# Optimization experiments

Measured on AMD Instinct MI355X. Metric: run time of the kernel, lower is better.

Reference implementation:

```python
import jax, jax.numpy as jnp
import numpy as np
import math

N, D, H, N_BINS, MAX_GRID = 4096, 512, 4, 32, 40

def setup_inputs() -> dict:
    key = jax.random.key(0)
    ks = jax.random.split(key, 12)
    vision_h = jax.random.normal(ks[0], (N, D), dtype=jnp.float32)
    patch_rows = jax.random.randint(ks[1], (N,), 0, MAX_GRID, dtype=jnp.int32)
    patch_cols = jax.random.randint(ks[2], (N,), 0, MAX_GRID, dtype=jnp.int32)
    pos_w = 0.01 * jax.random.normal(ks[3], (D, D), dtype=jnp.float32)
    q_w = 0.02 * jax.random.normal(ks[4], (D, D), dtype=jnp.float32)
    k_w = 0.02 * jax.random.normal(ks[5], (D, D), dtype=jnp.float32)
    v_w = 0.02 * jax.random.normal(ks[6], (D, D), dtype=jnp.float32)
    out_w = 0.02 * jax.random.normal(ks[7], (D, D), dtype=jnp.float32)
    dist_bias = 0.02 * jax.random.normal(ks[8], (H, N_BINS), dtype=jnp.float32)
    gamma_param = jnp.array(0.5, dtype=jnp.float32)
    ln_w = jnp.ones((D,), dtype=jnp.float32)
    ln_b = jnp.zeros((D,), dtype=jnp.float32)
    return {"vision_h": vision_h, "patch_rows": patch_rows, "patch_cols": patch_cols,
            "pos_w": pos_w, "q_w": q_w, "k_w": k_w, "v_w": v_w, "out_w": out_w,
            "dist_bias": dist_bias, "gamma_param": gamma_param, "ln_w": ln_w, "ln_b": ln_b}

def _sin_pe_1d(pos_f, half_dim):
    # pos_f: (N,) float. returns (N, half_dim) with even idx = sin, odd idx = cos
    freq = jnp.exp(jnp.arange(0, half_dim, 2, dtype=jnp.float32) * (-(math.log(10000.0) / half_dim)))
    ang = pos_f[:, None] * freq  # (N, half_dim//2)
    return jnp.stack([jnp.sin(ang), jnp.cos(ang)], axis=-1).reshape(pos_f.shape[0], half_dim)

def reference(vision_h, patch_rows, patch_cols, pos_w, q_w, k_w, v_w, out_w,
              dist_bias, gamma_param, ln_w, ln_b):
    n, d = vision_h.shape
    h = dist_bias.shape[0]
    hd = d // h
    n_bins = dist_bias.shape[1]
    half = d // 2

    rows_f = patch_rows.astype(jnp.float32)
    cols_f = patch_cols.astype(jnp.float32)
    pe = jnp.concatenate([_sin_pe_1d(rows_f, half), _sin_pe_1d(cols_f, half)], axis=-1)  # (N, D)

    h_pos = vision_h + pe @ pos_w.T
    Q = (h_pos @ q_w.T).reshape(n, h, hd).transpose(1, 0, 2)   # (H, N, hd)
    K = (h_pos @ k_w.T).reshape(n, h, hd).transpose(1, 0, 2)
    V = (vision_h @ v_w.T).reshape(n, h, hd).transpose(1, 0, 2)

    logits = jnp.einsum("hnd,hmd->hnm", Q, K) / math.sqrt(hd)   # (H, N, N)

    row_diff = rows_f[:, None] - rows_f[None, :]
    col_diff = cols_f[:, None] - cols_f[None, :]
    dist = jnp.sqrt(row_diff ** 2 + col_diff ** 2)              # (N, N)
    max_log_dist = math.log1p(MAX_GRID * math.sqrt(2.0))
    bins = (jnp.log1p(dist) / max_log_dist * (n_bins - 1)).astype(jnp.int32)
    bins = jnp.clip(bins, 0, n_bins - 1)
    rel_bias = dist_bias[:, bins]                               # (H, N, N)

    attn = jax.nn.softmax(logits + rel_bias, axis=-1)
    attn_out = jnp.einsum("hnm,hmd->hnd", attn, V).transpose(1, 0, 2).reshape(n, d)

    o = attn_out @ out_w.T
    mu = jnp.mean(o, axis=-1, keepdims=True)
    var = jnp.mean((o - mu) ** 2, axis=-1, keepdims=True)
    o_ln = (o - mu) / jnp.sqrt(var + 1e-5) * ln_w + ln_b

    gamma = jax.nn.softplus(gamma_param)
    return vision_h + gamma * o_ln
```

## Files before the change

### kernel.cpp

```cpp
#include <hip/hip_runtime.h>
#include <math.h>

#define N_TOK 4096
#define DMODEL 512
#define NHEAD 4
#define HDIM 128
#define NBINS 32
#define BQ 128
#define BK 64
#define NSPLIT 4
#define KV_PER_SPLIT (N_TOK / NSPLIT)
#define QKSTR 1024
#define LOG2E 1.4426950408889634f

typedef __attribute__((ext_vector_type(8))) short bf16x8;
typedef __attribute__((ext_vector_type(4))) float f32x4;
typedef __attribute__((ext_vector_type(8))) unsigned short u16x8;
typedef __attribute__((ext_vector_type(4))) unsigned short u16x4;

__device__ __forceinline__ unsigned short f2bf(float x) {
    unsigned int u = __float_as_uint(x);
    u += 0x7FFFu + ((u >> 16) & 1u);
    return (unsigned short)(u >> 16);
}
__device__ __forceinline__ float bf2f(unsigned short u) {
    return __uint_as_float(((unsigned int)u) << 16);
}

__global__ __launch_bounds__(256) void pe_prep(const int* __restrict__ rows,
                                               const int* __restrict__ cols,
                                               const float* __restrict__ vh,
                                               unsigned short* __restrict__ pe_bf,
                                               unsigned short* __restrict__ vh_bf) {
    int n = blockIdx.x, t = threadIdx.x;
    float pos = (float)((t < 128) ? rows[n] : cols[n]);
    int k = t & 127;
    float freq = expf(-0.035977892078032f * (float)(2 * k));
    float ang = pos * freq;
    int base = n * DMODEL + ((t < 128) ? 0 : 256) + 2 * k;
    pe_bf[base]     = f2bf(sinf(ang));
    pe_bf[base + 1] = f2bf(cosf(ang));
    float2 v = *(const float2*)&vh[(size_t)n * DMODEL + t * 2];
    vh_bf[(size_t)n * DMODEL + t * 2]     = f2bf(v.x);
    vh_bf[(size_t)n * DMODEL + t * 2 + 1] = f2bf(v.y);
}

__global__ __launch_bounds__(256) void wconv5(const float* __restrict__ w0, const float* __restrict__ w1,
                                              const float* __restrict__ w2, const float* __restrict__ w3,
                                              const float* __restrict__ w4,
                                              unsigned short* __restrict__ dstbase) {
    const float* srcs[5] = {w0, w1, w2, w3, w4};
    const float* src = srcs[blockIdx.y];
    unsigned short* dst = dstbase + (size_t)blockIdx.y * DMODEL * DMODEL;
    int idx = (blockIdx.x * 256 + threadIdx.x) * 4;
    float4 v = *(const float4*)&src[idx];
    u16x4 r;
    r[0] = f2bf(v.x); r[1] = f2bf(v.y); r[2] = f2bf(v.z); r[3] = f2bf(v.w);
    *(u16x4*)&dst[idx] = r;
}

template <bool ADD, bool BF16OUT>
__global__ __launch_bounds__(256) void gemm_mfma(const unsigned short* __restrict__ A,
                                                 const unsigned short* __restrict__ B,
                                                 const float* __restrict__ addv,
                                                 void* __restrict__ Cv,
                                                 int M, int N, int K,
                                                 float scaleA, float scaleB) {
    const int n0 = blockIdx.x * 64;
    const int j0 = blockIdx.y * 128;
    __shared__ unsigned short As[64][72];
    __shared__ unsigned short Bs[128][72];
    const int t    = threadIdx.x;
    const int wid  = t >> 6;
    const int wr   = wid >> 1, wc = wid & 1;
    const int lane = t & 63;
    const int lg   = lane >> 4, li = lane & 15;
    const int str  = t >> 3;
    const int sc   = (t & 7) * 8;

    f32x4 acc[2][4];
#pragma unroll
    for (int i = 0; i < 2; ++i)
#pragma unroll
        for (int j = 0; j < 4; ++j) acc[i][j] = (f32x4){0.f, 0.f, 0.f, 0.f};

    u16x8 areg[2], breg[4];
#pragma unroll
    for (int i = 0; i < 2; ++i)
        areg[i] = *(const u16x8*)&A[(size_t)(n0 + str + i * 32) * K + sc];
#pragma unroll
    for (int i = 0; i < 4; ++i)
        breg[i] = *(const u16x8*)&B[(size_t)(j0 + str + i * 32) * K + sc];

    for (int k0 = 0; k0 < K; k0 += 64) {
        __syncthreads();
#pragma unroll
        for (int i = 0; i < 2; ++i) *(u16x8*)&As[str + i * 32][sc] = areg[i];
#pragma unroll
        for (int i = 0; i < 4; ++i) *(u16x8*)&Bs[str + i * 32][sc] = breg[i];
        __syncthreads();
        if (k0 + 64 < K) {
#pragma unroll
            for (int i = 0; i < 2; ++i)
                areg[i] = *(const u16x8*)&A[(size_t)(n0 + str + i * 32) * K + k0 + 64 + sc];
#pragma unroll
            for (int i = 0; i < 4; ++i)
                breg[i] = *(const u16x8*)&B[(size_t)(j0 + str + i * 32) * K + k0 + 64 + sc];
        }
        __builtin_amdgcn_s_setprio(1);
#pragma unroll
        for (int kc = 0; kc < 2; ++kc) {
            bf16x8 af[2], bfr[4];
#pragma unroll
            for (int mf = 0; mf < 2; ++mf)
                af[mf] = *(const bf16x8*)&As[wr * 32 + mf * 16 + li][kc * 32 + lg * 8];
#pragma unroll
            for (int nf = 0; nf < 4; ++nf)
                bfr[nf] = *(const bf16x8*)&Bs[wc * 64 + nf * 16 + li][kc * 32 + lg * 8];
#pragma unroll
            for (int mf = 0; mf < 2; ++mf)
#pragma unroll
                for (int nf = 0; nf < 4; ++nf)
                    acc[mf][nf] = __builtin_amdgcn_mfma_f32_16x16x32_bf16(af[mf], bfr[nf], acc[mf][nf], 0, 0, 0);
        }
        __builtin_amdgcn_s_setprio(0);
    }
    const float scl = (j0 < 512) ? scaleA : scaleB;
#pragma unroll
    for (int mf = 0; mf < 2; ++mf) {
#pragma unroll
        for (int r = 0; r < 4; ++r) {
            const int row = n0 + wr * 32 + mf * 16 + lg * 4 + r;
#pragma unroll
            for (int nf = 0; nf < 4; ++nf) {
                const int col = j0 + wc * 64 + nf * 16 + li;
                float v = acc[mf][nf][r] * scl;
                if (ADD) v += addv[(size_t)row * N + col];
                if (BF16OUT) ((unsigned short*)Cv)[(size_t)row * N + col] = f2bf(v);
                else         ((float*)Cv)[(size_t)row * N + col] = v;
            }
        }
    }
}

__global__ __launch_bounds__(512, 2) void attn_mfma(const unsigned short* __restrict__ Qb,
                                                    const unsigned short* __restrict__ Kb,
                                                    const unsigned short* __restrict__ Vtb,
                                                    const int* __restrict__ prows,
                                                    const int* __restrict__ pcols,
                                                    const float* __restrict__ dist_bias,
                                                    unsigned short* __restrict__ Opart,
                                                    float* __restrict__ Mp,
                                                    float* __restrict__ Lp) {
    const int h  = blockIdx.y;
    const int n0 = blockIdx.x * BQ;
    const int sp = blockIdx.z;
    __shared__ unsigned short Ks[BK * HDIM];
    __shared__ unsigned short Vts[HDIM * BK];
    __shared__ unsigned short Ps[BQ][68];
    __shared__ unsigned short biasTb[6241];
    __shared__ int klins[BK];

    const int t    = threadIdx.x;
    const int lane = t & 63;
    const int lg   = lane >> 4;
    const int li   = lane & 15;
    const int qbase = (t >> 6) * 16;

    for (int idx = t; idx < 6241; idx += 512) {
        int dr = idx / 79 - 39;
        int dc = idx % 79 - 39;
        float d  = sqrtf((float)(dr * dr + dc * dc));
        int bin  = (int)(log1pf(d) * (31.0f / 4.0529789877f));
        bin = bin > 31 ? 31 : bin;
        biasTb[idx] = f2bf(dist_bias[h * NBINS + bin] * LOG2E);
    }

    bf16x8 qf[4];
    {
        const unsigned short* qptr = &Qb[(size_t)(n0 + qbase + li) * QKSTR + h * HDIM];
#pragma unroll
        for (int kc = 0; kc < 4; ++kc)
            qf[kc] = *(const bf16x8*)&qptr[kc * 32 + lg * 8];
    }
    const int qlin3 = prows[n0 + qbase + li] * 79 + pcols[n0 + qbase + li] + 3120;

    float m_ = -1e30f;
    float l_ = 0.f;
    f32x4 accO[8];
#pragma unroll
    for (int dt = 0; dt < 8; ++dt) accO[dt] = (f32x4){0.f, 0.f, 0.f, 0.f};

    u16x8 kreg[2], vreg[2];
    int klinreg = 0;
    const int ktr = t >> 4, kch = (t & 15) * 8;
    const int vtr = t >> 3, vch = (t & 7) * 8;

    const int kwofs0 = (ktr * 128 + kch) * 2;
    const int vwofs0 = (vtr * 64 + vch) * 2;

    int m0 = sp * KV_PER_SPLIT;
    {
#pragma unroll
        for (int i = 0; i < 2; ++i)
            kreg[i] = *(const u16x8*)&Kb[(size_t)(m0 + ktr + i * 32) * QKSTR + h * HDIM + kch];
#pragma unroll
        for (int i = 0; i < 2; ++i)
            vreg[i] = *(const u16x8*)&Vtb[(size_t)(h * HDIM + vtr + i * 64) * N_TOK + m0 + vch];
        if (t < BK) klinreg = prows[m0 + t] * 79 + pcols[m0 + t];
    }

    for (int kb = 0; kb < KV_PER_SPLIT / BK; ++kb, m0 += BK) {
        __syncthreads();
#pragma unroll
        for (int i = 0; i < 2; ++i) {
            int ofs = (kwofs0 + i * 32 * 256) ^ ((ktr & 7) << 4);
            *(u16x8*)((char*)Ks + ofs) = kreg[i];
        }
#pragma unroll
        for (int i = 0; i < 2; ++i) {
            int ofs = (vwofs0 + i * 64 * 128) ^ ((vtr & 7) << 4);
            *(u16x8*)((char*)Vts + ofs) = vreg[i];
        }
        if (t < BK) klins[t] = klinreg;
        __syncthreads();

        if (kb + 1 < KV_PER_SPLIT / BK) {
            const int m1 = m0 + BK;
#pragma unroll
            for (int i = 0; i < 2; ++i)
                kreg[i] = *(const u16x8*)&Kb[(size_t)(m1 + ktr + i * 32) * QKSTR + h * HDIM + kch];
#pragma unroll
            for (int i = 0; i < 2; ++i)
                vreg[i] = *(const u16x8*)&Vtb[(size_t)(h * HDIM + vtr + i * 64) * N_TOK + m1 + vch];
            if (t < BK) klinreg = prows[m1 + t] * 79 + pcols[m1 + t];
        }

        f32x4 s[4];
        __builtin_amdgcn_s_setprio(1);
#pragma unroll
        for (int jt = 0; jt < 4; ++jt) {
            f32x4 acc = {0.f, 0.f, 0.f, 0.f};
#pragma unroll
            for (int kc = 0; kc < 4; ++kc) {
                int ofs = (((jt * 16 + li) * 128 + kc * 32 + lg * 8) * 2) ^ ((li & 7) << 4);
                bf16x8 kf = *(const bf16x8*)((const char*)Ks + ofs);
                acc = __builtin_amdgcn_mfma_f32_16x16x32_bf16(kf, qf[kc], acc, 0, 0, 0);
            }
            s[jt] = acc;
        }
        __builtin_amdgcn_s_setprio(0);

        float p[4][4];
#pragma unroll
        for (int jt = 0; jt < 4; ++jt) {
#pragma unroll
            for (int r = 0; r < 4; ++r) {
                int k = jt * 16 + lg * 4 + r;
                p[jt][r] = s[jt][r] + bf2f(biasTb[qlin3 - klins[k]]);
            }
        }

        float t0 = fmaxf(fmaxf(p[0][0], p[0][1]), fmaxf(p[0][2], p[0][3]));
        float t1 = fmaxf(fmaxf(p[1][0], p[1][1]), fmaxf(p[1][2], p[1][3]));
        float t2 = fmaxf(fmaxf(p[2][0], p[2][1]), fmaxf(p[2][2], p[2][3]));
        float t3 = fmaxf(fmaxf(p[3][0], p[3][1]), fmaxf(p[3][2], p[3][3]));
        float pmax = fmaxf(fmaxf(t0, t1), fmaxf(t2, t3));
        pmax = fmaxf(pmax, __shfl_xor(pmax, 16));
        pmax = fmaxf(pmax, __shfl_xor(pmax, 32));

        if (!__all(pmax <= m_ + 11.5415603f)) {
            float mnew  = fmaxf(m_, pmax);
            float alpha = __builtin_amdgcn_exp2f(m_ - mnew);
            m_ = mnew;
            l_ *= alpha;
            float aq[4];
#pragma unroll
            for (int r = 0; r < 4; ++r)
                aq[r] = __shfl(alpha, (lane & 48) | (lg * 4 + r));
#pragma unroll
            for (int dt = 0; dt < 8; ++dt)
#pragma unroll
                for (int r = 0; r < 4; ++r) accO[dt][r] *= aq[r];
        }

        float rs = 0.f;
#pragma unroll
        for (int jt = 0; jt < 4; ++jt)
#pragma unroll
            for (int r = 0; r < 4; ++r) {
                p[jt][r] = __builtin_amdgcn_exp2f(p[jt][r] - m_);
                rs += p[jt][r];
            }
        rs += __shfl_xor(rs, 16);
        rs += __shfl_xor(rs, 32);
        l_ += rs;

#pragma unroll
        for (int jt = 0; jt < 4; ++jt) {
            u16x4 w;
#pragma unroll
            for (int r = 0; r < 4; ++r) w[r] = f2bf(p[jt][r]);
            *(u16x4*)&Ps[qbase + li][jt * 16 + lg * 4] = w;
        }

        bf16x8 pf0 = *(const bf16x8*)&Ps[qbase + li][lg * 8];
        bf16x8 pf1 = *(const bf16x8*)&Ps[qbase + li][32 + lg * 8];
        __builtin_amdgcn_s_setprio(1);
#pragma unroll
        for (int dt = 0; dt < 8; ++dt) {
            int ofs0 = (((dt * 16 + li) * 64 + lg * 8) * 2) ^ ((li & 7) << 4);
            bf16x8 vf0 = *(const bf16x8*)((const char*)Vts + ofs0);
            bf16x8 vf1 = *(const bf16x8*)((const char*)Vts + (ofs0 ^ 64));
            accO[dt] = __builtin_amdgcn_mfma_f32_16x16x32_bf16(pf0, vf0, accO[dt], 0, 0, 0);
            accO[dt] = __builtin_amdgcn_mfma_f32_16x16x32_bf16(pf1, vf1, accO[dt], 0, 0, 0);
        }
        __builtin_amdgcn_s_setprio(0);
    }

    float linv[4];
#pragma unroll
    for (int r = 0; r < 4; ++r)
        linv[r] = __shfl(l_, (lane & 48) | (lg * 4 + r));
#pragma unroll
    for (int r = 0; r < 4; ++r) {
        float inv = 1.0f / linv[r];
        int row = n0 + qbase + lg * 4 + r;
#pragma unroll
        for (int dt = 0; dt < 8; ++dt)
            Opart[(size_t)sp * N_TOK * DMODEL + (size_t)row * DMODEL + h * HDIM + dt * 16 + li] =
                f2bf(accO[dt][r] * inv);
    }
    if (lane < 16) {
        int row = n0 + qbase + lane;
        Mp[((size_t)sp * NHEAD + h) * N_TOK + row] = m_;
        Lp[((size_t)sp * NHEAD + h) * N_TOK + row] = l_;
    }
}

__global__ __launch_bounds__(256) void combine_kernel(const unsigned short* __restrict__ Opart,
                                                      const float* __restrict__ Mp,
                                                      const float* __restrict__ Lp,
                                                      unsigned short* __restrict__ outbf) {
    int n = blockIdx.x, t = threadIdx.x;
#pragma unroll
    for (int d0 = t; d0 < DMODEL; d0 += 256) {
        int h = d0 >> 7;
        float mm[NSPLIT], ll[NSPLIT];
        float m = -1e30f;
#pragma unroll
        for (int s = 0; s < NSPLIT; ++s) {
            mm[s] = Mp[((size_t)s * NHEAD + h) * N_TOK + n];
            ll[s] = Lp[((size_t)s * NHEAD + h) * N_TOK + n];
            m = fmaxf(m, mm[s]);
        }
        float acc = 0.f, lsum = 0.f;
#pragma unroll
        for (int s = 0; s < NSPLIT; ++s) {
            float a = __builtin_amdgcn_exp2f(mm[s] - m) * ll[s];
            lsum += a;
            acc += a * bf2f(Opart[(size_t)s * N_TOK * DMODEL + (size_t)n * DMODEL + d0]);
        }
        outbf[(size_t)n * DMODEL + d0] = f2bf(acc / lsum);
    }
}

__global__ __launch_bounds__(256) void final_kernel(const float* __restrict__ o,
                                                    const float* __restrict__ vh,
                                                    const float* __restrict__ lnw,
                                                    const float* __restrict__ lnb,
                                                    const float* __restrict__ gparam,
                                                    float* __restrict__ out) {
    int n = blockIdx.x, t = threadIdx.x;
    size_t base = (size_t)n * DMODEL;
    float x0 = o[base + t], x1 = o[base + t + 256];
    __shared__ float red[4];
    float v = x0 + x1;
#pragma unroll
    for (int off = 32; off > 0; off >>= 1) v += __shfl_down(v, off, 64);
    if ((t & 63) == 0) red[t >> 6] = v;
    __syncthreads();
    float mu = (red[0] + red[1] + red[2] + red[3]) * (1.0f / 512.0f);
    __syncthreads();
    float d0 = x0 - mu, d1 = x1 - mu;
    v = d0 * d0 + d1 * d1;
#pragma unroll
    for (int off = 32; off > 0; off >>= 1) v += __shfl_down(v, off, 64);
    if ((t & 63) == 0) red[t >> 6] = v;
    __syncthreads();
    float var  = (red[0] + red[1] + red[2] + red[3]) * (1.0f / 512.0f);
    float rstd = rsqrtf(var + 1e-5f);
    float gamma = log1pf(expf(gparam[0]));
    out[base + t]       = vh[base + t]       + gamma * (d0 * rstd * lnw[t]       + lnb[t]);
    out[base + t + 256] = vh[base + t + 256] + gamma * (d1 * rstd * lnw[t + 256] + lnb[t + 256]);
}

extern "C" void kernel_launch(void* const* d_in, const int* in_sizes, int n_in,
                              void* d_out, int out_size, void* d_ws, size_t ws_size,
                              hipStream_t stream) {
    const float* vision_h  = (const float*)d_in[0];
    const int*   prows     = (const int*)d_in[1];
    const int*   pcols     = (const int*)d_in[2];
    const float* pos_w     = (const float*)d_in[3];
    const float* q_w       = (const float*)d_in[4];
    const float* k_w       = (const float*)d_in[5];
    const float* v_w       = (const float*)d_in[6];
    const float* out_w     = (const float*)d_in[7];
    const float* dist_bias = (const float*)d_in[8];
    const float* gamma_p   = (const float*)d_in[9];
    const float* ln_w      = (const float*)d_in[10];
    const float* ln_b      = (const float*)d_in[11];
    float* out = (float*)d_out;
    char* base = (char*)d_ws;

    const size_t MB = 1024 * 1024;
    unsigned short* pe_bf   = (unsigned short*)(base + 0);
    unsigned short* vh_bf   = (unsigned short*)(base + 4  * MB);
    unsigned short* hpos_bf = (unsigned short*)(base + 8  * MB);
    unsigned short* Opart   = (unsigned short*)(base + 0);
    float*          ob      = (float*)(base + 0);
    unsigned short* QKb     = (unsigned short*)(base + 16 * MB);
    unsigned short* Vtb     = (unsigned short*)(base + 24 * MB);
    unsigned short* attn_bf = (unsigned short*)(base + 28 * MB);
    float*          Mp      = (float*)(base + 32 * MB);
    float*          Lp      = (float*)(base + 32 * MB + 262144);
    unsigned short* wbf     = (unsigned short*)(base + 32 * MB + 524288);

    unsigned short* w_pos = wbf;
    unsigned short* w_q   = wbf + 1 * DMODEL * DMODEL;
    unsigned short* w_v   = wbf + 3 * DMODEL * DMODEL;
    unsigned short* w_o   = wbf + 4 * DMODEL * DMODEL;

    const float qscale = 0.08838834764831845f * LOG2E;

    pe_prep<<<N_TOK, 256, 0, stream>>>(prows, pcols, vision_h, pe_bf, vh_bf);
    wconv5<<<dim3(256, 5), 256, 0, stream>>>(pos_w, q_w, k_w, v_w, out_w, wbf);
    gemm_mfma<true,  true ><<<dim3(64, 4), 256, 0, stream>>>(pe_bf, w_pos, vision_h, hpos_bf,
                                                             N_TOK, DMODEL, DMODEL, 1.0f, 1.0f);
    gemm_mfma<false, true ><<<dim3(64, 8), 256, 0, stream>>>(hpos_bf, w_q, nullptr, QKb,
                                                             N_TOK, 1024, DMODEL, qscale, 1.0f);
    gemm_mfma<false, true ><<<dim3(8, 32), 256, 0, stream>>>(w_v, vh_bf, nullptr, Vtb,
                                                             DMODEL, N_TOK, DMODEL, 1.0f, 1.0f);
    attn_mfma<<<dim3(N_TOK / BQ, NHEAD, NSPLIT), 512, 0, stream>>>(QKb, QKb + 512, Vtb, prows, pcols,
                                                                   dist_bias, Opart, Mp, Lp);
    combine_kernel<<<N_TOK, 256, 0, stream>>>(Opart, Mp, Lp, attn_bf);
    gemm_mfma<false, false><<<dim3(64, 4), 256, 0, stream>>>(attn_bf, w_o, nullptr, ob,
                                                             N_TOK, DMODEL, DMODEL, 1.0f, 1.0f);
    final_kernel<<<N_TOK, 256, 0, stream>>>(ob, vision_h, ln_w, ln_b, gamma_p, out);
}
```

Before: 149.4 us.

## Read K/V fragments directly from global memory in attention, drop LDS staging

The attention kernel stops staging K and V tiles through shared memory with register prefetch and barriers. Each wave now loads its MFMA operand fragments straight from global memory, relying on L1/L2 reuse. The query tile is halved to 64 with 256-thread blocks, and a precomputed linear patch index replaces the row/col loads, with key indices broadcast by shuffle instead of LDS. Per-iteration barriers and LDS traffic go away, at the cost of uncoalesced, redundant global loads per wave and twice as many blocks that each rebuild the bias table.

```diff
diff --git a/kernel.cpp b/kernel.cpp
--- a/kernel.cpp
+++ b/kernel.cpp
@@ -6,7 +6,7 @@
 #define NHEAD 4
 #define HDIM 128
 #define NBINS 32
-#define BQ 128
+#define BQ 64
 #define BK 64
 #define NSPLIT 4
 #define KV_PER_SPLIT (N_TOK / NSPLIT)
@@ -31,7 +31,8 @@
                                                const int* __restrict__ cols,
                                                const float* __restrict__ vh,
                                                unsigned short* __restrict__ pe_bf,
-                                               unsigned short* __restrict__ vh_bf) {
+                                               unsigned short* __restrict__ vh_bf,
+                                               int* __restrict__ plin) {
     int n = blockIdx.x, t = threadIdx.x;
     float pos = (float)((t < 128) ? rows[n] : cols[n]);
     int k = t & 127;
@@ -43,6 +44,7 @@
     float2 v = *(const float2*)&vh[(size_t)n * DMODEL + t * 2];
     vh_bf[(size_t)n * DMODEL + t * 2]     = f2bf(v.x);
     vh_bf[(size_t)n * DMODEL + t * 2 + 1] = f2bf(v.y);
+    if (t == 0) plin[n] = rows[n] * 79 + cols[n];
 }
 
 __global__ __launch_bounds__(256) void wconv5(const float* __restrict__ w0, const float* __restrict__ w1,
@@ -143,23 +145,19 @@
     }
 }
 
-__global__ __launch_bounds__(512, 2) void attn_mfma(const unsigned short* __restrict__ Qb,
-                                                    const unsigned short* __restrict__ Kb,
-                                                    const unsigned short* __restrict__ Vtb,
-                                                    const int* __restrict__ prows,
-                                                    const int* __restrict__ pcols,
-                                                    const float* __restrict__ dist_bias,
-                                                    unsigned short* __restrict__ Opart,
-                                                    float* __restrict__ Mp,
-                                                    float* __restrict__ Lp) {
+__global__ __launch_bounds__(256) void attn_mfma(const unsigned short* __restrict__ Qb,
+                                                 const unsigned short* __restrict__ Kb,
+                                                 const unsigned short* __restrict__ Vtb,
+                                                 const int* __restrict__ plin,
+                                                 const float* __restrict__ dist_bias,
+                                                 unsigned short* __restrict__ Opart,
+                                                 float* __restrict__ Mp,
+                                                 float* __restrict__ Lp) {
     const int h  = blockIdx.y;
     const int n0 = blockIdx.x * BQ;
     const int sp = blockIdx.z;
-    __shared__ unsigned short Ks[BK * HDIM];
-    __shared__ unsigned short Vts[HDIM * BK];
     __shared__ unsigned short Ps[BQ][68];
     __shared__ unsigned short biasTb[6241];
-    __shared__ int klins[BK];
 
     const int t    = threadIdx.x;
     const int lane = t & 63;
@@ -167,7 +165,7 @@
     const int li   = lane & 15;
     const int qbase = (t >> 6) * 16;
 
-    for (int idx = t; idx < 6241; idx += 512) {
+    for (int idx = t; idx < 6241; idx += 256) {
         int dr = idx / 79 - 39;
         int dc = idx % 79 - 39;
         float d  = sqrtf((float)(dr * dr + dc * dc));
@@ -183,7 +181,8 @@
         for (int kc = 0; kc < 4; ++kc)
             qf[kc] = *(const bf16x8*)&qptr[kc * 32 + lg * 8];
     }
-    const int qlin3 = prows[n0 + qbase + li] * 79 + pcols[n0 + qbase + li] + 3120;
+    const int qlin3 = plin[n0 + qbase + li] + 3120;
+    __syncthreads();
 
     float m_ = -1e30f;
     float l_ = 0.f;
@@ -191,50 +190,12 @@
 #pragma unroll
     for (int dt = 0; dt < 8; ++dt) accO[dt] = (f32x4){0.f, 0.f, 0.f, 0.f};
 
-    u16x8 kreg[2], vreg[2];
-    int klinreg = 0;
-    const int ktr = t >> 4, kch = (t & 15) * 8;
-    const int vtr = t >> 3, vch = (t & 7) * 8;
-
-    const int kwofs0 = (ktr * 128 + kch) * 2;
-    const int vwofs0 = (vtr * 64 + vch) * 2;
+    const unsigned short* Kh = Kb + h * HDIM;
+    const unsigned short* Vh = Vtb + (size_t)h * HDIM * N_TOK;
 
     int m0 = sp * KV_PER_SPLIT;
-    {
-#pragma unroll
-        for (int i = 0; i < 2; ++i)
-            kreg[i] = *(const u16x8*)&Kb[(size_t)(m0 + ktr + i * 32) * QKSTR + h * HDIM + kch];
-#pragma unroll
-        for (int i = 0; i < 2; ++i)
-            vreg[i] = *(const u16x8*)&Vtb[(size_t)(h * HDIM + vtr + i * 64) * N_TOK + m0 + vch];
-        if (t < BK) klinreg = prows[m0 + t] * 79 + pcols[m0 + t];
-    }
-
     for (int kb = 0; kb < KV_PER_SPLIT / BK; ++kb, m0 += BK) {
-        __syncthreads();
-#pragma unroll
-        for (int i = 0; i < 2; ++i) {
-            int ofs = (kwofs0 + i * 32 * 256) ^ ((ktr & 7) << 4);
-            *(u16x8*)((char*)Ks + ofs) = kreg[i];
-        }
-#pragma unroll
-        for (int i = 0; i < 2; ++i) {
-            int ofs = (vwofs0 + i * 64 * 128) ^ ((vtr & 7) << 4);
-            *(u16x8*)((char*)Vts + ofs) = vreg[i];
-        }
-        if (t < BK) klins[t] = klinreg;
-        __syncthreads();
-
-        if (kb + 1 < KV_PER_SPLIT / BK) {
-            const int m1 = m0 + BK;
-#pragma unroll
-            for (int i = 0; i < 2; ++i)
-                kreg[i] = *(const u16x8*)&Kb[(size_t)(m1 + ktr + i * 32) * QKSTR + h * HDIM + kch];
-#pragma unroll
-            for (int i = 0; i < 2; ++i)
-                vreg[i] = *(const u16x8*)&Vtb[(size_t)(h * HDIM + vtr + i * 64) * N_TOK + m1 + vch];
-            if (t < BK) klinreg = prows[m1 + t] * 79 + pcols[m1 + t];
-        }
+        const int myklin = plin[m0 + lane];
 
         f32x4 s[4];
         __builtin_amdgcn_s_setprio(1);
@@ -243,8 +204,7 @@
             f32x4 acc = {0.f, 0.f, 0.f, 0.f};
 #pragma unroll
             for (int kc = 0; kc < 4; ++kc) {
-                int ofs = (((jt * 16 + li) * 128 + kc * 32 + lg * 8) * 2) ^ ((li & 7) << 4);
-                bf16x8 kf = *(const bf16x8*)((const char*)Ks + ofs);
+                bf16x8 kf = *(const bf16x8*)&Kh[(size_t)(m0 + jt * 16 + li) * QKSTR + kc * 32 + lg * 8];
                 acc = __builtin_amdgcn_mfma_f32_16x16x32_bf16(kf, qf[kc], acc, 0, 0, 0);
             }
             s[jt] = acc;
@@ -257,7 +217,7 @@
 #pragma unroll
             for (int r = 0; r < 4; ++r) {
                 int k = jt * 16 + lg * 4 + r;
-                p[jt][r] = s[jt][r] + bf2f(biasTb[qlin3 - klins[k]]);
+                p[jt][r] = s[jt][r] + bf2f(biasTb[qlin3 - __shfl(myklin, k)]);
             }
         }
 
@@ -303,15 +263,15 @@
             for (int r = 0; r < 4; ++r) w[r] = f2bf(p[jt][r]);
             *(u16x4*)&Ps[qbase + li][jt * 16 + lg * 4] = w;
         }
-
         bf16x8 pf0 = *(const bf16x8*)&Ps[qbase + li][lg * 8];
         bf16x8 pf1 = *(const bf16x8*)&Ps[qbase + li][32 + lg * 8];
+
         __builtin_amdgcn_s_setprio(1);
 #pragma unroll
         for (int dt = 0; dt < 8; ++dt) {
-            int ofs0 = (((dt * 16 + li) * 64 + lg * 8) * 2) ^ ((li & 7) << 4);
-            bf16x8 vf0 = *(const bf16x8*)((const char*)Vts + ofs0);
-            bf16x8 vf1 = *(const bf16x8*)((const char*)Vts + (ofs0 ^ 64));
+            const unsigned short* vrow = &Vh[(size_t)(dt * 16 + li) * N_TOK + m0];
+            bf16x8 vf0 = *(const bf16x8*)&vrow[lg * 8];
+            bf16x8 vf1 = *(const bf16x8*)&vrow[32 + lg * 8];
             accO[dt] = __builtin_amdgcn_mfma_f32_16x16x32_bf16(pf0, vf0, accO[dt], 0, 0, 0);
             accO[dt] = __builtin_amdgcn_mfma_f32_16x16x32_bf16(pf1, vf1, accO[dt], 0, 0, 0);
         }
@@ -425,6 +385,7 @@
     float*          Mp      = (float*)(base + 32 * MB);
     float*          Lp      = (float*)(base + 32 * MB + 262144);
     unsigned short* wbf     = (unsigned short*)(base + 32 * MB + 524288);
+    int*            plin    = (int*)(base + 35 * MB);
 
     unsigned short* w_pos = wbf;
     unsigned short* w_q   = wbf + 1 * DMODEL * DMODEL;
@@ -433,7 +394,7 @@
 
     const float qscale = 0.08838834764831845f * LOG2E;
 
-    pe_prep<<<N_TOK, 256, 0, stream>>>(prows, pcols, vision_h, pe_bf, vh_bf);
+    pe_prep<<<N_TOK, 256, 0, stream>>>(prows, pcols, vision_h, pe_bf, vh_bf, plin);
     wconv5<<<dim3(256, 5), 256, 0, stream>>>(pos_w, q_w, k_w, v_w, out_w, wbf);
     gemm_mfma<true,  true ><<<dim3(64, 4), 256, 0, stream>>>(pe_bf, w_pos, vision_h, hpos_bf,
                                                              N_TOK, DMODEL, DMODEL, 1.0f, 1.0f);
@@ -441,7 +402,7 @@
                                                              N_TOK, 1024, DMODEL, qscale, 1.0f);
     gemm_mfma<false, true ><<<dim3(8, 32), 256, 0, stream>>>(w_v, vh_bf, nullptr, Vtb,
                                                              DMODEL, N_TOK, DMODEL, 1.0f, 1.0f);
-    attn_mfma<<<dim3(N_TOK / BQ, NHEAD, NSPLIT), 512, 0, stream>>>(QKb, QKb + 512, Vtb, prows, pcols,
+    attn_mfma<<<dim3(N_TOK / BQ, NHEAD, NSPLIT), 256, 0, stream>>>(QKb, QKb + 512, Vtb, plin,
                                                                    dist_bias, Opart, Mp, Lp);
     combine_kernel<<<N_TOK, 256, 0, stream>>>(Opart, Mp, Lp, attn_bf);
     gemm_mfma<false, false><<<dim3(64, 4), 256, 0, stream>>>(attn_bf, w_o, nullptr, ob,
```

Result: slower. 355.8 us (+138.2%).

## Process two query tiles per wave and precompute bias LUT globally

Applied to the files above, without the earlier changes.

The attention kernel moves from 512 threads with 16 query rows per wave to 256 threads with 32 query rows per wave. Each K fragment loaded from LDS now feeds two MFMAs, and each V fragment feeds four, which halves LDS reads per FLOP. The per-block distance-bias table computation is moved into a separate bias_lut kernel, and the linearised patch positions are precomputed in pe_prep, so attention blocks only copy the table. In exchange, register pressure roughly doubles (two accO sets), there are fewer waves per block to hide latency, and one extra kernel launch is added.

```diff
diff --git a/kernel.cpp b/kernel.cpp
--- a/kernel.cpp
+++ b/kernel.cpp
@@ -12,6 +12,8 @@
 #define KV_PER_SPLIT (N_TOK / NSPLIT)
 #define QKSTR 1024
 #define LOG2E 1.4426950408889634f
+#define LUTN 6241
+#define LUTP 6256
 
 typedef __attribute__((ext_vector_type(8))) short bf16x8;
 typedef __attribute__((ext_vector_type(4))) float f32x4;
@@ -31,7 +33,8 @@
                                                const int* __restrict__ cols,
                                                const float* __restrict__ vh,
                                                unsigned short* __restrict__ pe_bf,
-                                               unsigned short* __restrict__ vh_bf) {
+                                               unsigned short* __restrict__ vh_bf,
+                                               int* __restrict__ plin) {
     int n = blockIdx.x, t = threadIdx.x;
     float pos = (float)((t < 128) ? rows[n] : cols[n]);
     int k = t & 127;
@@ -43,6 +46,21 @@
     float2 v = *(const float2*)&vh[(size_t)n * DMODEL + t * 2];
     vh_bf[(size_t)n * DMODEL + t * 2]     = f2bf(v.x);
     vh_bf[(size_t)n * DMODEL + t * 2 + 1] = f2bf(v.y);
+    if (t == 0) plin[n] = rows[n] * 79 + cols[n];
+}
+
+__global__ __launch_bounds__(256) void bias_lut(const float* __restrict__ dist_bias,
+                                                unsigned short* __restrict__ biasG) {
+    int h = blockIdx.y;
+    int idx = blockIdx.x * 256 + threadIdx.x;
+    if (idx >= LUTP) return;
+    int i = idx < LUTN ? idx : LUTN - 1;
+    int dr = i / 79 - 39;
+    int dc = i % 79 - 39;
+    float d  = sqrtf((float)(dr * dr + dc * dc));
+    int bin  = (int)(log1pf(d) * (31.0f / 4.0529789877f));
+    bin = bin > 31 ? 31 : bin;
+    biasG[h * LUTP + idx] = f2bf(dist_bias[h * NBINS + bin] * LOG2E);
 }
 
 __global__ __launch_bounds__(256) void wconv5(const float* __restrict__ w0, const float* __restrict__ w1,
@@ -143,55 +161,52 @@
     }
 }
 
-__global__ __launch_bounds__(512, 2) void attn_mfma(const unsigned short* __restrict__ Qb,
-                                                    const unsigned short* __restrict__ Kb,
-                                                    const unsigned short* __restrict__ Vtb,
-                                                    const int* __restrict__ prows,
-                                                    const int* __restrict__ pcols,
-                                                    const float* __restrict__ dist_bias,
-                                                    unsigned short* __restrict__ Opart,
-                                                    float* __restrict__ Mp,
-                                                    float* __restrict__ Lp) {
+__global__ __launch_bounds__(256) void attn_mfma(const unsigned short* __restrict__ Qb,
+                                                 const unsigned short* __restrict__ Kb,
+                                                 const unsigned short* __restrict__ Vtb,
+                                                 const int* __restrict__ plin,
+                                                 const unsigned short* __restrict__ biasG,
+                                                 unsigned short* __restrict__ Opart,
+                                                 float* __restrict__ Mp,
+                                                 float* __restrict__ Lp) {
     const int h  = blockIdx.y;
     const int n0 = blockIdx.x * BQ;
     const int sp = blockIdx.z;
     __shared__ unsigned short Ks[BK * HDIM];
     __shared__ unsigned short Vts[HDIM * BK];
     __shared__ unsigned short Ps[BQ][68];
-    __shared__ unsigned short biasTb[6241];
+    __shared__ unsigned short biasTb[LUTP];
     __shared__ int klins[BK];
 
     const int t    = threadIdx.x;
     const int lane = t & 63;
     const int lg   = lane >> 4;
     const int li   = lane & 15;
-    const int qbase = (t >> 6) * 16;
-
-    for (int idx = t; idx < 6241; idx += 512) {
-        int dr = idx / 79 - 39;
-        int dc = idx % 79 - 39;
-        float d  = sqrtf((float)(dr * dr + dc * dc));
-        int bin  = (int)(log1pf(d) * (31.0f / 4.0529789877f));
-        bin = bin > 31 ? 31 : bin;
-        biasTb[idx] = f2bf(dist_bias[h * NBINS + bin] * LOG2E);
-    }
-
-    bf16x8 qf[4];
-    {
-        const unsigned short* qptr = &Qb[(size_t)(n0 + qbase + li) * QKSTR + h * HDIM];
+    const int qbase = (t >> 6) * 32;
+
+    for (int idx = t; idx < LUTP / 8; idx += 256)
+        *(u16x8*)&biasTb[idx * 8] = *(const u16x8*)&biasG[h * LUTP + idx * 8];
+
+    bf16x8 qf[2][4];
+    int qlin3[2];
+#pragma unroll
+    for (int iq = 0; iq < 2; ++iq) {
+        const unsigned short* qptr = &Qb[(size_t)(n0 + qbase + iq * 16 + li) * QKSTR + h * HDIM];
 #pragma unroll
         for (int kc = 0; kc < 4; ++kc)
-            qf[kc] = *(const bf16x8*)&qptr[kc * 32 + lg * 8];
-    }
-    const int qlin3 = prows[n0 + qbase + li] * 79 + pcols[n0 + qbase + li] + 3120;
-
-    float m_ = -1e30f;
-    float l_ = 0.f;
-    f32x4 accO[8];
-#pragma unroll
-    for (int dt = 0; dt < 8; ++dt) accO[dt] = (f32x4){0.f, 0.f, 0.f, 0.f};
-
-    u16x8 kreg[2], vreg[2];
+            qf[iq][kc] = *(const bf16x8*)&qptr[kc * 32 + lg * 8];
+        qlin3[iq] = plin[n0 + qbase + iq * 16 + li] + 3120;
+    }
+
+    float m_[2] = {-1e30f, -1e30f};
+    float l_[2] = {0.f, 0.f};
+    f32x4 accO[2][8];
+#pragma unroll
+    for (int iq = 0; iq < 2; ++iq)
+#pragma unroll
+        for (int dt = 0; dt < 8; ++dt) accO[iq][dt] = (f32x4){0.f, 0.f, 0.f, 0.f};
+
+    u16x8 kreg[4], vreg[4];
     int klinreg = 0;
     const int ktr = t >> 4, kch = (t & 15) * 8;
     const int vtr = t >> 3, vch = (t & 7) * 8;
@@ -202,24 +217,24 @@
     int m0 = sp * KV_PER_SPLIT;
     {
 #pragma unroll
-        for (int i = 0; i < 2; ++i)
-            kreg[i] = *(const u16x8*)&Kb[(size_t)(m0 + ktr + i * 32) * QKSTR + h * HDIM + kch];
-#pragma unroll
-        for (int i = 0; i < 2; ++i)
-            vreg[i] = *(const u16x8*)&Vtb[(size_t)(h * HDIM + vtr + i * 64) * N_TOK + m0 + vch];
-        if (t < BK) klinreg = prows[m0 + t] * 79 + pcols[m0 + t];
+        for (int i = 0; i < 4; ++i)
+            kreg[i] = *(const u16x8*)&Kb[(size_t)(m0 + ktr + i * 16) * QKSTR + h * HDIM + kch];
+#pragma unroll
+        for (int i = 0; i < 4; ++i)
+            vreg[i] = *(const u16x8*)&Vtb[(size_t)(h * HDIM + vtr + i * 32) * N_TOK + m0 + vch];
+        if (t < BK) klinreg = plin[m0 + t];
     }
 
     for (int kb = 0; kb < KV_PER_SPLIT / BK; ++kb, m0 += BK) {
         __syncthreads();
 #pragma unroll
-        for (int i = 0; i < 2; ++i) {
-            int ofs = (kwofs0 + i * 32 * 256) ^ ((ktr & 7) << 4);
+        for (int i = 0; i < 4; ++i) {
+            int ofs = (kwofs0 + i * 16 * 256) ^ ((ktr & 7) << 4);
             *(u16x8*)((char*)Ks + ofs) = kreg[i];
         }
 #pragma unroll
-        for (int i = 0; i < 2; ++i) {
-            int ofs = (vwofs0 + i * 64 * 128) ^ ((vtr & 7) << 4);
+        for (int i = 0; i < 4; ++i) {
+            int ofs = (vwofs0 + i * 32 * 128) ^ ((vtr & 7) << 4);
             *(u16x8*)((char*)Vts + ofs) = vreg[i];
         }
         if (t < BK) klins[t] = klinreg;
@@ -228,113 +243,130 @@
         if (kb + 1 < KV_PER_SPLIT / BK) {
             const int m1 = m0 + BK;
 #pragma unroll
-            for (int i = 0; i < 2; ++i)
-                kreg[i] = *(const u16x8*)&Kb[(size_t)(m1 + ktr + i * 32) * QKSTR + h * HDIM + kch];
-#pragma unroll
-            for (int i = 0; i < 2; ++i)
-                vreg[i] = *(const u16x8*)&Vtb[(size_t)(h * HDIM + vtr + i * 64) * N_TOK + m1 + vch];
-            if (t < BK) klinreg = prows[m1 + t] * 79 + pcols[m1 + t];
-        }
-
-        f32x4 s[4];
+            for (int i = 0; i < 4; ++i)
+                kreg[i] = *(const u16x8*)&Kb[(size_t)(m1 + ktr + i * 16) * QKSTR + h * HDIM + kch];
+#pragma unroll
+            for (int i = 0; i < 4; ++i)
+                vreg[i] = *(const u16x8*)&Vtb[(size_t)(h * HDIM + vtr + i * 32) * N_TOK + m1 + vch];
+            if (t < BK) klinreg = plin[m1 + t];
+        }
+
+        int kl[4][4];
+#pragma unroll
+        for (int jt = 0; jt < 4; ++jt)
+#pragma unroll
+            for (int r = 0; r < 4; ++r) kl[jt][r] = klins[jt * 16 + lg * 4 + r];
+
+        f32x4 s[4][2];
         __builtin_amdgcn_s_setprio(1);
 #pragma unroll
         for (int jt = 0; jt < 4; ++jt) {
-            f32x4 acc = {0.f, 0.f, 0.f, 0.f};
+            f32x4 a0 = {0.f, 0.f, 0.f, 0.f}, a1 = {0.f, 0.f, 0.f, 0.f};
 #pragma unroll
             for (int kc = 0; kc < 4; ++kc) {
                 int ofs = (((jt * 16 + li) * 128 + kc * 32 + lg * 8) * 2) ^ ((li & 7) << 4);
                 bf16x8 kf = *(const bf16x8*)((const char*)Ks + ofs);
-                acc = __builtin_amdgcn_mfma_f32_16x16x32_bf16(kf, qf[kc], acc, 0, 0, 0);
+                a0 = __builtin_amdgcn_mfma_f32_16x16x32_bf16(kf, qf[0][kc], a0, 0, 0, 0);
+                a1 = __builtin_amdgcn_mfma_f32_16x16x32_bf16(kf, qf[1][kc], a1, 0, 0, 0);
             }
-            s[jt] = acc;
+            s[jt][0] = a0; s[jt][1] = a1;
         }
         __builtin_amdgcn_s_setprio(0);
 
-        float p[4][4];
-#pragma unroll
-        for (int jt = 0; jt < 4; ++jt) {
-#pragma unroll
-            for (int r = 0; r < 4; ++r) {
-                int k = jt * 16 + lg * 4 + r;
-                p[jt][r] = s[jt][r] + bf2f(biasTb[qlin3 - klins[k]]);
+#pragma unroll
+        for (int iq = 0; iq < 2; ++iq) {
+            float p[4][4];
+#pragma unroll
+            for (int jt = 0; jt < 4; ++jt)
+#pragma unroll
+                for (int r = 0; r < 4; ++r)
+                    p[jt][r] = s[jt][iq][r] + bf2f(biasTb[qlin3[iq] - kl[jt][r]]);
+
+            float t0 = fmaxf(fmaxf(p[0][0], p[0][1]), fmaxf(p[0][2], p[0][3]));
+            float t1 = fmaxf(fmaxf(p[1][0], p[1][1]), fmaxf(p[1][2], p[1][3]));
+            float t2 = fmaxf(fmaxf(p[2][0], p[2][1]), fmaxf(p[2][2], p[2][3]));
+            float t3 = fmaxf(fmaxf(p[3][0], p[3][1]), fmaxf(p[3][2], p[3][3]));
+            float pmax = fmaxf(fmaxf(t0, t1), fmaxf(t2, t3));
+            pmax = fmaxf(pmax, __shfl_xor(pmax, 16));
+            pmax = fmaxf(pmax, __shfl_xor(pmax, 32));
+
+            if (!__all(pmax <= m_[iq] + 11.5415603f)) {
+                float mnew  = fmaxf(m_[iq], pmax);
+                float alpha = __builtin_amdgcn_exp2f(m_[iq] - mnew);
+                m_[iq] = mnew;
+                l_[iq] *= alpha;
+                float aq[4];
+#pragma unroll
+                for (int r = 0; r < 4; ++r)
+                    aq[r] = __shfl(alpha, (lane & 48) | (lg * 4 + r));
+#pragma unroll
+                for (int dt = 0; dt < 8; ++dt)
+#pragma unroll
+                    for (int r = 0; r < 4; ++r) accO[iq][dt][r] *= aq[r];
             }
-        }
-
-        float t0 = fmaxf(fmaxf(p[0][0], p[0][1]), fmaxf(p[0][2], p[0][3]));
-        float t1 = fmaxf(fmaxf(p[1][0], p[1][1]), fmaxf(p[1][2], p[1][3]));
-        float t2 = fmaxf(fmaxf(p[2][0], p[2][1]), fmaxf(p[2][2], p[2][3]));
-        float t3 = fmaxf(fmaxf(p[3][0], p[3][1]), fmaxf(p[3][2], p[3][3]));
-        float pmax = fmaxf(fmaxf(t0, t1), fmaxf(t2, t3));
-        pmax = fmaxf(pmax, __shfl_xor(pmax, 16));
-        pmax = fmaxf(pmax, __shfl_xor(pmax, 32));
-
-        if (!__all(pmax <= m_ + 11.5415603f)) {
-            float mnew  = fmaxf(m_, pmax);
-            float alpha = __builtin_amdgcn_exp2f(m_ - mnew);
-            m_ = mnew;
-            l_ *= alpha;
-            float aq[4];
-#pragma unroll
-            for (int r = 0; r < 4; ++r)
-                aq[r] = __shfl(alpha, (lane & 48) | (lg * 4 + r));
-#pragma unroll
-            for (int dt = 0; dt < 8; ++dt)
-#pragma unroll
-                for (int r = 0; r < 4; ++r) accO[dt][r] *= aq[r];
-        }
-
-        float rs = 0.f;
-#pragma unroll
-        for (int jt = 0; jt < 4; ++jt)
-#pragma unroll
-            for (int r = 0; r < 4; ++r) {
-                p[jt][r] = __builtin_amdgcn_exp2f(p[jt][r] - m_);
-                rs += p[jt][r];
+
+            float rs = 0.f;
+#pragma unroll
+            for (int jt = 0; jt < 4; ++jt)
+#pragma unroll
+                for (int r = 0; r < 4; ++r) {
+                    p[jt][r] = __builtin_amdgcn_exp2f(p[jt][r] - m_[iq]);
+                    rs += p[jt][r];
+                }
+            rs += __shfl_xor(rs, 16);
+            rs += __shfl_xor(rs, 32);
+            l_[iq] += rs;
+
+#pragma unroll
+            for (int jt = 0; jt < 4; ++jt) {
+                u16x4 w;
+#pragma unroll
+                for (int r = 0; r < 4; ++r) w[r] = f2bf(p[jt][r]);
+                *(u16x4*)&Ps[qbase + iq * 16 + li][jt * 16 + lg * 4] = w;
             }
-        rs += __shfl_xor(rs, 16);
-        rs += __shfl_xor(rs, 32);
-        l_ += rs;
-
-#pragma unroll
-        for (int jt = 0; jt < 4; ++jt) {
-            u16x4 w;
-#pragma unroll
-            for (int r = 0; r < 4; ++r) w[r] = f2bf(p[jt][r]);
-            *(u16x4*)&Ps[qbase + li][jt * 16 + lg * 4] = w;
-        }
-
-        bf16x8 pf0 = *(const bf16x8*)&Ps[qbase + li][lg * 8];
-        bf16x8 pf1 = *(const bf16x8*)&Ps[qbase + li][32 + lg * 8];
+        }
+
+        bf16x8 pf[2][2];
+#pragma unroll
+        for (int iq = 0; iq < 2; ++iq) {
+            pf[iq][0] = *(const bf16x8*)&Ps[qbase + iq * 16 + li][lg * 8];
+            pf[iq][1] = *(const bf16x8*)&Ps[qbase + iq * 16 + li][32 + lg * 8];
+        }
+
         __builtin_amdgcn_s_setprio(1);
 #pragma unroll
         for (int dt = 0; dt < 8; ++dt) {
             int ofs0 = (((dt * 16 + li) * 64 + lg * 8) * 2) ^ ((li & 7) << 4);
             bf16x8 vf0 = *(const bf16x8*)((const char*)Vts + ofs0);
             bf16x8 vf1 = *(const bf16x8*)((const char*)Vts + (ofs0 ^ 64));
-            accO[dt] = __builtin_amdgcn_mfma_f32_16x16x32_bf16(pf0, vf0, accO[dt], 0, 0, 0);
-            accO[dt] = __builtin_amdgcn_mfma_f32_16x16x32_bf16(pf1, vf1, accO[dt], 0, 0, 0);
+            accO[0][dt] = __builtin_amdgcn_mfma_f32_16x16x32_bf16(pf[0][0], vf0, accO[0][dt], 0, 0, 0);
+            accO[0][dt] = __builtin_amdgcn_mfma_f32_16x16x32_bf16(pf[0][1], vf1, accO[0][dt], 0, 0, 0);
+            accO[1][dt] = __builtin_amdgcn_mfma_f32_16x16x32_bf16(pf[1][0], vf0, accO[1][dt], 0, 0, 0);
+            accO[1][dt] = __builtin_amdgcn_mfma_f32_16x16x32_bf16(pf[1][1], vf1, accO[1][dt], 0, 0, 0);
         }
         __builtin_amdgcn_s_setprio(0);
     }
 
-    float linv[4];
-#pragma unroll
-    for (int r = 0; r < 4; ++r)
-        linv[r] = __shfl(l_, (lane & 48) | (lg * 4 + r));
-#pragma unroll
-    for (int r = 0; r < 4; ++r) {
-        float inv = 1.0f / linv[r];
-        int row = n0 + qbase + lg * 4 + r;
-#pragma unroll
-        for (int dt = 0; dt < 8; ++dt)
-            Opart[(size_t)sp * N_TOK * DMODEL + (size_t)row * DMODEL + h * HDIM + dt * 16 + li] =
-                f2bf(accO[dt][r] * inv);
-    }
-    if (lane < 16) {
-        int row = n0 + qbase + lane;
-        Mp[((size_t)sp * NHEAD + h) * N_TOK + row] = m_;
-        Lp[((size_t)sp * NHEAD + h) * N_TOK + row] = l_;
+#pragma unroll
+    for (int iq = 0; iq < 2; ++iq) {
+        float linv[4];
+#pragma unroll
+        for (int r = 0; r < 4; ++r)
+            linv[r] = __shfl(l_[iq], (lane & 48) | (lg * 4 + r));
+#pragma unroll
+        for (int r = 0; r < 4; ++r) {
+            float inv = 1.0f / linv[r];
+            int row = n0 + qbase + iq * 16 + lg * 4 + r;
+#pragma unroll
+            for (int dt = 0; dt < 8; ++dt)
+                Opart[(size_t)sp * N_TOK * DMODEL + (size_t)row * DMODEL + h * HDIM + dt * 16 + li] =
+                    f2bf(accO[iq][dt][r] * inv);
+        }
+        if (lane < 16) {
+            int row = n0 + qbase + iq * 16 + lane;
+            Mp[((size_t)sp * NHEAD + h) * N_TOK + row] = m_[iq];
+            Lp[((size_t)sp * NHEAD + h) * N_TOK + row] = l_[iq];
+        }
     }
 }
 
@@ -425,6 +457,8 @@
     float*          Mp      = (float*)(base + 32 * MB);
     float*          Lp      = (float*)(base + 32 * MB + 262144);
     unsigned short* wbf     = (unsigned short*)(base + 32 * MB + 524288);
+    int*            plin    = (int*)(base + 35 * MB);
+    unsigned short* biasG   = (unsigned short*)(base + 35 * MB + 65536);
 
     unsigned short* w_pos = wbf;
     unsigned short* w_q   = wbf + 1 * DMODEL * DMODEL;
@@ -433,7 +467,8 @@
 
     const float qscale = 0.08838834764831845f * LOG2E;
 
-    pe_prep<<<N_TOK, 256, 0, stream>>>(prows, pcols, vision_h, pe_bf, vh_bf);
+    pe_prep<<<N_TOK, 256, 0, stream>>>(prows, pcols, vision_h, pe_bf, vh_bf, plin);
+    bias_lut<<<dim3((LUTP + 255) / 256, NHEAD), 256, 0, stream>>>(dist_bias, biasG);
     wconv5<<<dim3(256, 5), 256, 0, stream>>>(pos_w, q_w, k_w, v_w, out_w, wbf);
     gemm_mfma<true,  true ><<<dim3(64, 4), 256, 0, stream>>>(pe_bf, w_pos, vision_h, hpos_bf,
                                                              N_TOK, DMODEL, DMODEL, 1.0f, 1.0f);
@@ -441,8 +476,8 @@
                                                              N_TOK, 1024, DMODEL, qscale, 1.0f);
     gemm_mfma<false, true ><<<dim3(8, 32), 256, 0, stream>>>(w_v, vh_bf, nullptr, Vtb,
                                                              DMODEL, N_TOK, DMODEL, 1.0f, 1.0f);
-    attn_mfma<<<dim3(N_TOK / BQ, NHEAD, NSPLIT), 512, 0, stream>>>(QKb, QKb + 512, Vtb, prows, pcols,
-                                                                   dist_bias, Opart, Mp, Lp);
+    attn_mfma<<<dim3(N_TOK / BQ, NHEAD, NSPLIT), 256, 0, stream>>>(QKb, QKb + 512, Vtb, plin,
+                                                                   biasG, Opart, Mp, Lp);
     combine_kernel<<<N_TOK, 256, 0, stream>>>(Opart, Mp, Lp, attn_bf);
     gemm_mfma<false, false><<<dim3(64, 4), 256, 0, stream>>>(attn_bf, w_o, nullptr, ob,
                                                              N_TOK, DMODEL, DMODEL, 1.0f, 1.0f);
```

Result: slower. 158.4 us (+6.0%).
